# Performance work log

Hardware: AMD Instinct MI355X
Metric: run time of the kernel (lower is better)

## Reference

```python
import jax, jax.numpy as jnp
import numpy as np

L, E, M, H, MAXT, V = 8, 1024, 4096, 16, 1024, 128
C = E // H  # head size = 64
EPS = 1e-5  # torch LayerNorm default


def layer_norm(x, g, b):
    mu = jnp.mean(x, axis=-1, keepdims=True)
    var = jnp.mean((x - mu) ** 2, axis=-1, keepdims=True)
    return (x - mu) * jax.lax.rsqrt(var + EPS) * g + b


def setup_inputs() -> dict:
    key = jax.random.key(0)
    ks = jax.random.split(key, 16)
    s = lambda *sh: 0.02
    return {
        "bytes_": jax.random.randint(ks[0], (2, 1024), 0, V),
        "W_tok": jax.random.normal(ks[1], (E, V), jnp.float32) * 0.02,      # token_embedding.weight
        "W_pos": jax.random.normal(ks[2], (E, MAXT), jnp.float32) * 0.02,    # postn_embedding.weight
        "Wqkv": jax.random.normal(ks[3], (L, 3 * E, E), jnp.float32) * 0.02,
        "ln1_g": jnp.ones((L, E), jnp.float32),
        "ln1_b": jnp.zeros((L, E), jnp.float32),
        "ln2_g": jnp.ones((L, E), jnp.float32),
        "ln2_b": jnp.zeros((L, E), jnp.float32),
        "W1": jax.random.normal(ks[4], (L, M, E), jnp.float32) * 0.02,
        "b1": jnp.zeros((L, M), jnp.float32),
        "W2": jax.random.normal(ks[5], (L, E, M), jnp.float32) * 0.02,
        "b2": jnp.zeros((L, E), jnp.float32),
        "lnf_g": jnp.ones((E,), jnp.float32),
        "lnf_b": jnp.zeros((E,), jnp.float32),
        "W_out": jax.random.normal(ks[6], (V, E), jnp.float32) * 0.02,
        "b_out": jnp.zeros((V,), jnp.float32),
    }


def _forward(bytes_, W_tok, W_pos, Wqkv, ln1_g, ln1_b, ln2_g, ln2_b,
             W1, b1, W2, b2, lnf_g, lnf_b, W_out, b_out):
    B, T = bytes_.shape
    # one-hot(bytes) @ W_tok.T == row-gather of W_tok.T
    x = jnp.take(W_tok.T, bytes_, axis=0) + W_pos.T[:T]  # [B,T,E]
    causal = jnp.tril(jnp.ones((T, T), bool))
    neg_inf = jnp.float32(-jnp.inf)

    def block(x, p):
        Wqkv_l, g1, b1n, g2, b2n, W1_l, b1_l, W2_l, b2_l = p
        h = layer_norm(x, g1, b1n)
        qkv = jnp.einsum('bte,fe->btf', h, Wqkv_l).reshape(B, T, H, 3 * C)
        q, k, v = jnp.split(qkv, 3, axis=-1)  # each [B,T,H,C]
        scores = jnp.einsum('bthc,bshc->bhts', q, k) / jnp.sqrt(jnp.float32(C))
        scores = jnp.where(causal, scores, neg_inf)  # + log(tril)
        probs = jax.nn.softmax(scores, axis=-1)
        y = jnp.einsum('bhts,bshc->bthc', probs, v).reshape(B, T, E)
        xb = x + y
        h2 = layer_norm(xb, g2, b2n)
        m = jax.nn.relu(jnp.einsum('bte,me->btm', h2, W1_l) + b1_l)
        m = jnp.einsum('btm,em->bte', m, W2_l) + b2_l
        xb = xb + m
        return x + xb, None  # extra outer residual: x = x + block(x)

    params = (Wqkv, ln1_g, ln1_b, ln2_g, ln2_b, W1, b1, W2, b2)
    x, _ = jax.lax.scan(block, x, params)
    h = layer_norm(x, lnf_g, lnf_b)
    return jnp.einsum('bte,ve->btv', h, W_out) + b_out  # [B,T,128]


def reference(bytes_, W_tok, W_pos, Wqkv, ln1_g, ln1_b, ln2_g, ln2_b,
              W1, b1, W2, b2, lnf_g, lnf_b, W_out, b_out):
    return _forward(bytes_, W_tok, W_pos, Wqkv, ln1_g, ln1_b, ln2_g, ln2_b,
                    W1, b1, W2, b2, lnf_g, lnf_b, W_out, b_out)
```

## Files before the change

### kernel.cpp

```cpp
#include <hip/hip_runtime.h>
#include <hip/hip_bf16.h>


typedef __bf16 bf16x8 __attribute__((ext_vector_type(8)));
typedef __bf16 bf16x4 __attribute__((ext_vector_type(4)));
typedef float  f32x4  __attribute__((ext_vector_type(4)));

#define DEV __device__ __forceinline__

DEV void load_lds16(const void* g, void* l) {
  __builtin_amdgcn_global_load_lds((const __attribute__((address_space(1))) void*)g,
                                   (__attribute__((address_space(3))) void*)l,
                                   16, 0, 0);
}

__global__ __launch_bounds__(256) void embed_k(const int* __restrict__ bytes,
                                               const float* __restrict__ Wtok,
                                               const float* __restrict__ Wpos,
                                               float* __restrict__ x) {
  const int row = blockIdx.x;
  const int t = row & 1023;
  const int byte = bytes[row];
  const int e0 = threadIdx.x * 4;
  f32x4 v;
#pragma unroll
  for (int j = 0; j < 4; ++j)
    v[j] = Wtok[(e0 + j) * 128 + byte] + Wpos[(e0 + j) * 1024 + t];
  *(f32x4*)(x + (long)row * 1024 + e0) = v;
}

__global__ __launch_bounds__(256) void cvt_k(const float* __restrict__ in,
                                             __bf16* __restrict__ out, int n4) {
  int i = blockIdx.x * 256 + threadIdx.x;
  if (i >= n4) return;
  f32x4 v = ((const f32x4*)in)[i];
  bf16x4 o = {(__bf16)v[0], (__bf16)v[1], (__bf16)v[2], (__bf16)v[3]};
  ((bf16x4*)out)[i] = o;
}

__global__ __launch_bounds__(256) void cvt3_k(const float* __restrict__ a,
                                              const float* __restrict__ b,
                                              const float* __restrict__ c,
                                              __bf16* __restrict__ oa,
                                              __bf16* __restrict__ ob,
                                              __bf16* __restrict__ oc) {
  int i = blockIdx.x * 256 + threadIdx.x;
  const float* s; __bf16* d; int off;
  if (i < 786432)                { s = a; d = oa; off = i; }
  else if (i < 786432 + 1048576) { s = b; d = ob; off = i - 786432; }
  else                           { s = c; d = oc; off = i - (786432 + 1048576); }
  f32x4 v = ((const f32x4*)s)[off];
  bf16x4 o = {(__bf16)v[0], (__bf16)v[1], (__bf16)v[2], (__bf16)v[3]};
  ((bf16x4*)d)[off] = o;
}

template <bool ADD>
__global__ __launch_bounds__(256) void ln_k(const float* __restrict__ xin,
                                            const float* __restrict__ yin,
                                            const float* __restrict__ g,
                                            const float* __restrict__ be,
                                            __bf16* __restrict__ hout,
                                            float* __restrict__ xbout) {
  const int row = blockIdx.x, tid = threadIdx.x;
  f32x4 v = ((const f32x4*)(xin + (long)row * 1024))[tid];
  if (ADD) v += ((const f32x4*)(yin + (long)row * 1024))[tid];
  float s  = v[0] + v[1] + v[2] + v[3];
  float ss = v[0]*v[0] + v[1]*v[1] + v[2]*v[2] + v[3]*v[3];
#pragma unroll
  for (int d = 1; d < 64; d <<= 1) { s += __shfl_xor(s, d, 64); ss += __shfl_xor(ss, d, 64); }
  __shared__ float red[4][2];
  const int w = tid >> 6;
  if ((tid & 63) == 0) { red[w][0] = s; red[w][1] = ss; }
  __syncthreads();
  s  = red[0][0] + red[1][0] + red[2][0] + red[3][0];
  ss = red[0][1] + red[1][1] + red[2][1] + red[3][1];
  const float mu  = s * (1.f / 1024.f);
  const float var = ss * (1.f / 1024.f) - mu * mu;
  const float rstd = rsqrtf(var + 1e-5f);
  f32x4 gv = ((const f32x4*)g)[tid];
  f32x4 bv = ((const f32x4*)be)[tid];
  f32x4 nv = (v - mu) * rstd * gv + bv;
  bf16x4 o = {(__bf16)nv[0], (__bf16)nv[1], (__bf16)nv[2], (__bf16)nv[3]};
  ((bf16x4*)(hout + (long)row * 1024))[tid] = o;
  if (ADD) ((f32x4*)(xbout + (long)row * 1024))[tid] = v;
}

template <int EPI, int SPLITK>
__global__ __launch_bounds__(256) void gemm_k(const __bf16* __restrict__ A,
                                              const __bf16* __restrict__ Bw,
                                              const float* __restrict__ bias,
                                              __bf16* __restrict__ outb,
                                              float* __restrict__ partial,
                                              int M, int N, int K) {
  const int tid = threadIdx.x;
  const int w = tid >> 6, l = tid & 63;
  const int bm = blockIdx.x, bn = blockIdx.y, bz = blockIdx.z;
  __shared__ __align__(16) __bf16 lA[2][4096];
  __shared__ __align__(16) __bf16 lB[2][4096];
  const f32x4 zero = {0.f, 0.f, 0.f, 0.f};
  f32x4 acc[4][4];
#pragma unroll
  for (int a = 0; a < 4; ++a)
#pragma unroll
    for (int b = 0; b < 4; ++b) acc[a][b] = zero;
  const int Kc = K / SPLITK;
  const int srow = w * 16 + (l >> 2);
  const int scol = (l & 3) * 8;
  const __bf16* Ap = A + (long)(bm * 128 + srow) * K + bz * Kc + scol;
  const __bf16* Bp = Bw + (long)(bn * 128 + srow) * K + bz * Kc + scol;
  const long rstr = (long)64 * K;
  const int lwoff = w * 512;
  const int lr = l & 15;
  const int kk = (l >> 4) * 8;
  const int mrow = (w >> 1) * 64, ncol = (w & 1) * 64;

#define STAGE(buf, kt)                                        \
  do {                                                        \
    load_lds16(Ap + (kt), &lA[buf][lwoff]);                   \
    load_lds16(Ap + (kt) + rstr, &lA[buf][lwoff + 2048]);     \
    load_lds16(Bp + (kt), &lB[buf][lwoff]);                   \
    load_lds16(Bp + (kt) + rstr, &lB[buf][lwoff + 2048]);     \
  } while (0)

  STAGE(0, 0);
  __syncthreads();
  int cur = 0;
  for (int kt = 0; kt < Kc; kt += 32) {
    if (kt + 32 < Kc) STAGE(cur ^ 1, kt + 32);
    bf16x8 af[4], bfv[4];
#pragma unroll
    for (int mi = 0; mi < 4; ++mi) af[mi] = *(const bf16x8*)&lA[cur][(mrow + mi * 16 + lr) * 32 + kk];
#pragma unroll
    for (int ni = 0; ni < 4; ++ni) bfv[ni] = *(const bf16x8*)&lB[cur][(ncol + ni * 16 + lr) * 32 + kk];
#pragma unroll
    for (int mi = 0; mi < 4; ++mi)
#pragma unroll
      for (int ni = 0; ni < 4; ++ni)
        acc[mi][ni] = __builtin_amdgcn_mfma_f32_16x16x32_bf16(af[mi], bfv[ni], acc[mi][ni], 0, 0, 0);
    __syncthreads();
    cur ^= 1;
  }
#undef STAGE
#pragma unroll
  for (int mi = 0; mi < 4; ++mi)
#pragma unroll
    for (int ni = 0; ni < 4; ++ni)
#pragma unroll
      for (int i = 0; i < 4; ++i) {
        const int r = bm * 128 + mrow + mi * 16 + (l >> 4) * 4 + i;
        const int c = bn * 128 + ncol + ni * 16 + lr;
        float v = acc[mi][ni][i];
        if (EPI == 0) {
          outb[(long)r * N + c] = (__bf16)v;
        } else if (EPI == 1) {
          v += bias[c];
          v = fmaxf(v, 0.f);
          outb[(long)r * N + c] = (__bf16)v;
        } else {
          partial[((long)bz * M + r) * N + c] = v;
        }
      }
}

__global__ __launch_bounds__(256) void attn_k(const __bf16* __restrict__ qkv,
                                              float* __restrict__ y) {
  const int qt = blockIdx.x;
  const int bh = blockIdx.y;
  const int bI = bh >> 4, h = bh & 15;
  const int tid = threadIdx.x, w = tid >> 6, l = tid & 63;
  const int lr = l & 15, kg = l >> 4;
  __shared__ __align__(16) __bf16 lK[32 * 64];
  __shared__ __align__(16) __bf16 lV[64 * 32];
  __shared__ __align__(16) __bf16 lP[4][16 * 32];
  const long base = (long)bI * 1024 * 3072;
  const __bf16* qp = qkv + base + (long)(qt * 64 + w * 16 + lr) * 3072 + h * 192;
  const bf16x8 qf0 = *(const bf16x8*)(qp + kg * 8);
  const bf16x8 qf1 = *(const bf16x8*)(qp + 32 + kg * 8);
  const f32x4 zero = {0.f, 0.f, 0.f, 0.f};
  f32x4 o[4] = {zero, zero, zero, zero};
  float mrow[4] = {-1e30f, -1e30f, -1e30f, -1e30f};
  float lsum[4] = {0.f, 0.f, 0.f, 0.f};
  const int qg = qt * 64 + w * 16 + kg * 4;
  const int nkt = 2 * qt + 2;
  const int srow = tid >> 3, sc = (tid & 7) * 8;
  for (int it = 0; it < nkt; ++it) {
    const int kt = it * 32;
    __syncthreads();
    {
      const __bf16* kp = qkv + base + (long)(kt + srow) * 3072 + h * 192 + 64 + sc;
      *(f32x4*)&lK[srow * 64 + sc] = *(const f32x4*)kp;
      bf16x8 vv = *(const bf16x8*)(kp + 64);
#pragma unroll
      for (int j = 0; j < 8; ++j) lV[(sc + j) * 32 + srow] = vv[j];
    }
    __syncthreads();
    f32x4 s0 = zero, s1 = zero;
    {
      bf16x8 k00 = *(const bf16x8*)&lK[lr * 64 + kg * 8];
      bf16x8 k01 = *(const bf16x8*)&lK[lr * 64 + 32 + kg * 8];
      s0 = __builtin_amdgcn_mfma_f32_16x16x32_bf16(qf0, k00, s0, 0, 0, 0);
      s0 = __builtin_amdgcn_mfma_f32_16x16x32_bf16(qf1, k01, s0, 0, 0, 0);
      bf16x8 k10 = *(const bf16x8*)&lK[(16 + lr) * 64 + kg * 8];
      bf16x8 k11 = *(const bf16x8*)&lK[(16 + lr) * 64 + 32 + kg * 8];
      s1 = __builtin_amdgcn_mfma_f32_16x16x32_bf16(qf0, k10, s1, 0, 0, 0);
      s1 = __builtin_amdgcn_mfma_f32_16x16x32_bf16(qf1, k11, s1, 0, 0, 0);
    }
#pragma unroll
    for (int i = 0; i < 4; ++i) {
      float a = s0[i] * 0.125f, b = s1[i] * 0.125f;
      const int q_i = qg + i;
      if (kt + lr > q_i)      a = -1e30f;
      if (kt + 16 + lr > q_i) b = -1e30f;
      float mx = fmaxf(a, b);
#pragma unroll
      for (int d = 1; d < 16; d <<= 1) mx = fmaxf(mx, __shfl_xor(mx, d, 64));
      const float mn = fmaxf(mrow[i], mx);
      const float scl = __expf(mrow[i] - mn);
      const float p0 = __expf(a - mn);
      const float p1 = __expf(b - mn);
      float ps = p0 + p1;
#pragma unroll
      for (int d = 1; d < 16; d <<= 1) ps += __shfl_xor(ps, d, 64);
      lsum[i] = lsum[i] * scl + ps;
      mrow[i] = mn;
      o[0][i] *= scl; o[1][i] *= scl; o[2][i] *= scl; o[3][i] *= scl;
      lP[w][(kg * 4 + i) * 32 + lr] = (__bf16)p0;
      lP[w][(kg * 4 + i) * 32 + 16 + lr] = (__bf16)p1;
    }
    bf16x8 pf = *(const bf16x8*)&lP[w][lr * 32 + kg * 8];
#pragma unroll
    for (int cf = 0; cf < 4; ++cf) {
      bf16x8 vf = *(const bf16x8*)&lV[(cf * 16 + lr) * 32 + kg * 8];
      o[cf] = __builtin_amdgcn_mfma_f32_16x16x32_bf16(pf, vf, o[cf], 0, 0, 0);
    }
  }
  float* yp = y + ((long)bI * 1024 + qt * 64 + w * 16 + kg * 4) * 1024 + h * 64 + lr;
#pragma unroll
  for (int i = 0; i < 4; ++i) {
    const float inv = 1.0f / lsum[i];
#pragma unroll
    for (int cf = 0; cf < 4; ++cf)
      yp[(long)i * 1024 + cf * 16] = o[cf][i] * inv;
  }
}

__global__ __launch_bounds__(256) void red_mlp_k(const float* __restrict__ part,
                                                 float* __restrict__ x,
                                                 const float* __restrict__ xb,
                                                 const float* __restrict__ b2) {
  const int i = blockIdx.x * 256 + threadIdx.x;
  const f32x4* p = (const f32x4*)part;
  f32x4 v = ((const f32x4*)x)[i] + ((const f32x4*)xb)[i] + ((const f32x4*)b2)[i & 255]
          + p[i] + p[i + 524288] + p[i + 2 * 524288] + p[i + 3 * 524288];
  ((f32x4*)x)[i] = v;
}

__global__ __launch_bounds__(256) void red_out_k(const float* __restrict__ part,
                                                 const float* __restrict__ bo,
                                                 float* __restrict__ out) {
  const int i = blockIdx.x * 256 + threadIdx.x;
  const f32x4* p = (const f32x4*)part;
  f32x4 v = ((const f32x4*)bo)[i & 31]
          + p[i] + p[i + 65536] + p[i + 2 * 65536] + p[i + 3 * 65536];
  ((f32x4*)out)[i] = v;
}

extern "C" void kernel_launch(void* const* d_in, const int* in_sizes, int n_in,
                              void* d_out, int out_size, void* d_ws, size_t ws_size,
                              hipStream_t stream) {
  (void)in_sizes; (void)n_in; (void)out_size; (void)ws_size;
  const int*   bytes = (const int*)  d_in[0];
  const float* Wtok  = (const float*)d_in[1];
  const float* Wpos  = (const float*)d_in[2];
  const float* Wqkv  = (const float*)d_in[3];
  const float* ln1g  = (const float*)d_in[4];
  const float* ln1b  = (const float*)d_in[5];
  const float* ln2g  = (const float*)d_in[6];
  const float* ln2b  = (const float*)d_in[7];
  const float* W1    = (const float*)d_in[8];
  const float* b1    = (const float*)d_in[9];
  const float* W2    = (const float*)d_in[10];
  const float* b2    = (const float*)d_in[11];
  const float* lnfg  = (const float*)d_in[12];
  const float* lnfb  = (const float*)d_in[13];
  const float* Wout  = (const float*)d_in[14];
  const float* bout  = (const float*)d_in[15];
  float* out = (float*)d_out;

  char* ws = (char*)d_ws;
  float*  x    = (float*) (ws + 0);
  float*  xb   = (float*) (ws + 8388608);
  float*  yb   = (float*) (ws + 16777216);
  __bf16* h    = (__bf16*)(ws + 25165824);
  __bf16* qkv  = (__bf16*)(ws + 29360128);
  __bf16* mb   = (__bf16*)(ws + 41943040);
  __bf16* wqb  = (__bf16*)(ws + 58720256);
  __bf16* w1b  = (__bf16*)(ws + 65011712);
  __bf16* w2b  = (__bf16*)(ws + 73400320);
  __bf16* wob  = (__bf16*)(ws + 81788928);
  float*  part = (float*) (ws + 82051072);

  embed_k<<<2048, 256, 0, stream>>>(bytes, Wtok, Wpos, x);
  cvt_k<<<128, 256, 0, stream>>>(Wout, wob, 32768);
  for (int lay = 0; lay < 8; ++lay) {
    cvt3_k<<<11264, 256, 0, stream>>>(Wqkv + (long)lay * 3145728,
                                      W1 + (long)lay * 4194304,
                                      W2 + (long)lay * 4194304, wqb, w1b, w2b);
    ln_k<false><<<2048, 256, 0, stream>>>(x, nullptr, ln1g + lay * 1024, ln1b + lay * 1024, h, nullptr);
    gemm_k<0, 1><<<dim3(16, 24, 1), 256, 0, stream>>>(h, wqb, nullptr, qkv, nullptr, 2048, 3072, 1024);
    attn_k<<<dim3(16, 32, 1), 256, 0, stream>>>(qkv, yb);
    ln_k<true><<<2048, 256, 0, stream>>>(x, yb, ln2g + lay * 1024, ln2b + lay * 1024, h, xb);
    gemm_k<1, 1><<<dim3(16, 32, 1), 256, 0, stream>>>(h, w1b, b1 + lay * 4096, mb, nullptr, 2048, 4096, 1024);
    gemm_k<2, 4><<<dim3(16, 8, 4), 256, 0, stream>>>(mb, w2b, nullptr, nullptr, part, 2048, 1024, 4096);
    red_mlp_k<<<2048, 256, 0, stream>>>(part, x, xb, b2 + lay * 1024);
  }
  ln_k<false><<<2048, 256, 0, stream>>>(x, nullptr, lnfg, lnfb, h, nullptr);
  gemm_k<2, 4><<<dim3(16, 1, 4), 256, 0, stream>>>(h, wob, nullptr, nullptr, part, 2048, 128, 1024);
  red_out_k<<<256, 256, 0, stream>>>(part, bout, out);
}
```

Before: 1.756 ms.

## Triple-buffer GEMM LDS tiles with explicit vmcnt waits for deeper prefetch

```diff
diff --git a/kernel.cpp b/kernel.cpp
--- a/kernel.cpp
+++ b/kernel.cpp
@@ -95,8 +95,8 @@
   const int tid = threadIdx.x;
   const int w = tid >> 6, l = tid & 63;
   const int bm = blockIdx.x, bn = blockIdx.y, bz = blockIdx.z;
-  __shared__ __align__(16) __bf16 lA[2][4096];
-  __shared__ __align__(16) __bf16 lB[2][4096];
+  __shared__ __align__(16) __bf16 lA[3][4096];
+  __shared__ __align__(16) __bf16 lB[3][4096];
   const f32x4 zero = {0.f, 0.f, 0.f, 0.f};
   f32x4 acc[4][4];
 #pragma unroll
@@ -104,6 +104,7 @@
 #pragma unroll
     for (int b = 0; b < 4; ++b) acc[a][b] = zero;
   const int Kc = K / SPLITK;
+  const int nt = Kc / 32;
   const int srow = w * 16 + (l >> 2);
   const int scol = (l & 3) * 8;
   const __bf16* Ap = A + (long)(bm * 128 + srow) * K + bz * Kc + scol;
@@ -114,33 +115,53 @@
   const int kk = (l >> 4) * 8;
   const int mrow = (w >> 1) * 64, ncol = (w & 1) * 64;
 
-#define STAGE(buf, kt)                                        \
-  do {                                                        \
-    load_lds16(Ap + (kt), &lA[buf][lwoff]);                   \
-    load_lds16(Ap + (kt) + rstr, &lA[buf][lwoff + 2048]);     \
-    load_lds16(Bp + (kt), &lB[buf][lwoff]);                   \
-    load_lds16(Bp + (kt) + rstr, &lB[buf][lwoff + 2048]);     \
+#define STAGE(buf, kt)                                            \
+  do {                                                            \
+    load_lds16(Ap + (kt), &lA[buf][lwoff]);                       \
+    load_lds16(Ap + (kt) + rstr, &lA[buf][lwoff + 2048]);         \
+    load_lds16(Bp + (kt), &lB[buf][lwoff]);                       \
+    load_lds16(Bp + (kt) + rstr, &lB[buf][lwoff + 2048]);         \
   } while (0)
 
+#define COMPUTE(b)                                                             \
+  do {                                                                         \
+    bf16x8 af[4], bfv[4];                                                      \
+    _Pragma("unroll")                                                          \
+    for (int mi = 0; mi < 4; ++mi)                                             \
+      af[mi] = *(const bf16x8*)&lA[b][(mrow + mi * 16 + lr) * 32 + kk];        \
+    _Pragma("unroll")                                                          \
+    for (int ni = 0; ni < 4; ++ni)                                             \
+      bfv[ni] = *(const bf16x8*)&lB[b][(ncol + ni * 16 + lr) * 32 + kk];       \
+    _Pragma("unroll")                                                          \
+    for (int mi = 0; mi < 4; ++mi)                                             \
+      _Pragma("unroll")                                                        \
+      for (int ni = 0; ni < 4; ++ni)                                           \
+        acc[mi][ni] = __builtin_amdgcn_mfma_f32_16x16x32_bf16(af[mi], bfv[ni], \
+                                                              acc[mi][ni], 0, 0, 0); \
+  } while (0)
+
   STAGE(0, 0);
-  __syncthreads();
-  int cur = 0;
-  for (int kt = 0; kt < Kc; kt += 32) {
-    if (kt + 32 < Kc) STAGE(cur ^ 1, kt + 32);
-    bf16x8 af[4], bfv[4];
-#pragma unroll
-    for (int mi = 0; mi < 4; ++mi) af[mi] = *(const bf16x8*)&lA[cur][(mrow + mi * 16 + lr) * 32 + kk];
-#pragma unroll
-    for (int ni = 0; ni < 4; ++ni) bfv[ni] = *(const bf16x8*)&lB[cur][(ncol + ni * 16 + lr) * 32 + kk];
-#pragma unroll
-    for (int mi = 0; mi < 4; ++mi)
-#pragma unroll
-      for (int ni = 0; ni < 4; ++ni)
-        acc[mi][ni] = __builtin_amdgcn_mfma_f32_16x16x32_bf16(af[mi], bfv[ni], acc[mi][ni], 0, 0, 0);
-    __syncthreads();
-    cur ^= 1;
+  STAGE(1, 32);
+  int rb = 0;
+  int sb = 2;
+  for (int t = 0; t < nt - 2; ++t) {
+    STAGE(sb, (t + 2) * 32);
+    sb = (sb == 2) ? 0 : sb + 1;
+    asm volatile("s_waitcnt vmcnt(8)" ::: "memory");
+    __builtin_amdgcn_s_barrier();
+    COMPUTE(rb);
+    rb = (rb == 2) ? 0 : rb + 1;
+    __builtin_amdgcn_s_barrier();
   }
+  asm volatile("s_waitcnt vmcnt(4)" ::: "memory");
+  __builtin_amdgcn_s_barrier();
+  COMPUTE(rb);
+  rb = (rb == 2) ? 0 : rb + 1;
+  asm volatile("s_waitcnt vmcnt(0)" ::: "memory");
+  __builtin_amdgcn_s_barrier();
+  COMPUTE(rb);
 #undef STAGE
+#undef COMPUTE
 #pragma unroll
   for (int mi = 0; mi < 4; ++mi)
 #pragma unroll
```

After: 1.804 ms. 1.03x slower.
